# Optimization experiments

Hardware: AMD Instinct MI355X
Metric: run time of the kernel (lower is better)

The kernel has to match this reference:

```python
import math
import jax, jax.numpy as jnp
import numpy as np

B, P, DC, NB, H = 32768, 16, 128, 32, 256
BOUND = 10.0
MIN_W = 1e-5
MIN_H = 1e-5
MIN_D = 1e-5
L2PI = 0.5 * math.log(2.0 * math.pi)


def setup_inputs() -> dict:
    key = jax.random.key(0)
    k0, k1, k2, k3 = jax.random.split(key, 4)
    x = jax.random.normal(k0, (B, P, 4), jnp.float32)
    c = jax.random.normal(k1, (B, P, DC), jnp.float32)
    W1 = jax.random.normal(k2, (DC, H), jnp.float32) / np.float32(np.sqrt(DC))
    b1 = jnp.zeros((H,), jnp.float32)
    # small init so spline params start near-identity-ish (typical subnet init)
    W2 = jax.random.normal(k3, (H, 3 * NB + 1), jnp.float32) * np.float32(0.1 / np.sqrt(H))
    b2 = jnp.zeros((3 * NB + 1,), jnp.float32)
    return {"x": x, "c": c, "W1": W1, "b1": b1, "W2": W2, "b2": b2}


def _pad_left_zero(a):
    # pad a zero at the start of the last axis
    pads = [(0, 0)] * (a.ndim - 1) + [(1, 0)]
    return jnp.pad(a, pads)


def _rqs_forward(x, theta):
    """Unconstrained rational-quadratic spline, forward direction.
    x: (B, P); theta: (B, P, 3*NB+1). Returns (z, log|det|), each (B, P)."""
    left, right, bottom, top = -BOUND, BOUND, -BOUND, BOUND
    inside = (x >= left) & (x <= right)

    uw = theta[..., :NB]
    uh = theta[..., NB:2 * NB]
    ud = theta[..., 2 * NB:]  # (B, P, NB+1)

    widths = MIN_W + (1.0 - MIN_W * NB) * jax.nn.softmax(uw, axis=-1)
    cumw = (right - left) * _pad_left_zero(jnp.cumsum(widths, axis=-1)) + left
    cumw = cumw.at[..., 0].set(left).at[..., -1].set(right)
    widths = cumw[..., 1:] - cumw[..., :-1]

    heights = MIN_H + (1.0 - MIN_H * NB) * jax.nn.softmax(uh, axis=-1)
    cumh = (top - bottom) * _pad_left_zero(jnp.cumsum(heights, axis=-1)) + bottom
    cumh = cumh.at[..., 0].set(bottom).at[..., -1].set(top)
    heights = cumh[..., 1:] - cumh[..., :-1]

    derivs = MIN_D + jax.nn.softplus(ud)  # (B, P, NB+1)

    xs = jnp.clip(x, left, right)
    # bin search: index of the bin containing xs
    bin_idx = jnp.clip(jnp.sum(xs[..., None] >= cumw, axis=-1) - 1, 0, NB - 1)
    idx = bin_idx[..., None]

    def g(a):
        return jnp.take_along_axis(a, idx, axis=-1)[..., 0]

    in_cw = g(cumw[..., :-1])
    in_w = g(widths)
    in_ch = g(cumh[..., :-1])
    in_h = g(heights)
    d0 = g(derivs[..., :-1])
    d1 = g(derivs[..., 1:])
    delta = in_h / in_w

    th = (xs - in_cw) / in_w
    th_om = th * (1.0 - th)
    numerator = in_h * (delta * th * th + d0 * th_om)
    denominator = delta + (d0 + d1 - 2.0 * delta) * th_om
    out = in_ch + numerator / denominator

    deriv_num = delta * delta * (d1 * th * th + 2.0 * delta * th_om + d0 * (1.0 - th) ** 2)
    logabsdet = jnp.log(deriv_num) - 2.0 * jnp.log(denominator)

    z = jnp.where(inside, out, x)
    jac = jnp.where(inside, logabsdet, jnp.zeros_like(x))
    return z, jac


def reference(x, c, W1, b1, W2, b2):
    # subnet MLP: c (B, P, DC) -> theta (B, P, 3*NB+1)
    h = jax.nn.relu(jnp.einsum("bpd,dh->bph", c, W1) + b1)
    theta = jnp.einsum("bph,hk->bpk", h, W2) + b2
    z, jac = _rqs_forward(x[..., -1], theta)
    prob = -L2PI - 0.5 * z * z + jac  # (B, P)
    return prob.sum(axis=1)  # (B,)
```

## Files before the change

### kernel.cpp

```cpp
#include <hip/hip_runtime.h>
#include <math.h>

#define NBLK 256
#define NTHR 512
#define PAIRS 8

typedef float  f32x4  __attribute__((ext_vector_type(4)));
typedef float  f32x16 __attribute__((ext_vector_type(16)));
typedef __bf16 bf16x8 __attribute__((ext_vector_type(8)));
typedef unsigned int u32x4 __attribute__((ext_vector_type(4)));

#define W1S 272
#define W2S 528
#define LDS_W1T 0
#define LDS_W2T 69632
#define LDS_B1  137216
#define LDS_B2  138240
#define LDS_TOTAL 138752

#define L2PIF 0.9189385332046727f
#define AW (1.0f - 32.0f*1e-5f)
#define LOG2E 1.4426950408889634f
#define LN2F  0.6931471805599453f

__device__ __forceinline__ void mfma_v(f32x16& acc, bf16x8 a, bf16x8 b) {
    asm("s_nop 1\n\tv_mfma_f32_32x32x16_bf16 %0, %1, %2, %0"
        : "+v"(acc) : "v"(a), "v"(b));
}
__device__ __forceinline__ void mfma_v_f(f32x16& acc, bf16x8 a, bf16x8 b) {
    asm("v_mfma_f32_32x32x16_bf16 %0, %1, %2, %0"
        : "+v"(acc) : "v"(a), "v"(b));
}
__device__ __forceinline__ void mfma_a_f(f32x16& acc, bf16x8 a, bf16x8 b) {
    asm("v_mfma_f32_32x32x16_bf16 %0, %1, %2, %0"
        : "+a"(acc) : "v"(a), "v"(b));
}
__device__ __forceinline__ void mfma_a_n(f32x16& acc, bf16x8 a, bf16x8 b) {
    asm("s_nop 1\n\tv_mfma_f32_32x32x16_bf16 %0, %1, %2, %0"
        : "+a"(acc) : "v"(a), "v"(b));
}
__device__ __forceinline__ void mfma_a_init(f32x16& acc, bf16x8 a, bf16x8 b) {
    asm("v_mfma_f32_32x32x16_bf16 %0, %1, %2, 0"
        : "=a"(acc) : "v"(a), "v"(b));
}
__device__ __forceinline__ void mfma_a_init_n(f32x16& acc, bf16x8 a, bf16x8 b) {
    asm("s_nop 1\n\tv_mfma_f32_32x32x16_bf16 %0, %1, %2, 0"
        : "=a"(acc) : "v"(a), "v"(b));
}
__device__ __forceinline__ void mfma_fence_va(f32x16& v0, f32x16& a1) {
    asm("s_nop 7\n\ts_nop 7\n\ts_nop 7" : "+v"(v0), "+a"(a1));
}
__device__ __forceinline__ void mfma_fence1(f32x16& a0) {
    asm("s_nop 7\n\ts_nop 7\n\ts_nop 7" : "+a"(a0));
}
__device__ __forceinline__ void mfma_fence2aa(f32x16& a0, f32x16& a1) {
    asm("s_nop 7\n\ts_nop 7\n\ts_nop 7" : "+a"(a0), "+a"(a1));
}

__device__ __forceinline__ void pl32swap(unsigned &a, unsigned &b) {
#if __has_builtin(__builtin_amdgcn_permlane32_swap)
    auto r = __builtin_amdgcn_permlane32_swap(a, b, false, false);
    a = (unsigned)r[0]; b = (unsigned)r[1];
#else
    asm("v_permlane32_swap_b32 %0, %1" : "+v"(a), "+v"(b));
#endif
}
__device__ __forceinline__ float sum32(float x) {
    unsigned a = __float_as_uint(x), b = a;
    pl32swap(a, b);
    return __uint_as_float(a) + __uint_as_float(b);
}
__device__ __forceinline__ float part32(float x) {
    unsigned u = __float_as_uint(x), a = u, b = u;
    pl32swap(a, b);
    return __uint_as_float(a ^ b ^ u);
}

__device__ __forceinline__ float rcpf(float x) {
#if __has_builtin(__builtin_amdgcn_rcpf)
    return __builtin_amdgcn_rcpf(x);
#else
    return 1.f / x;
#endif
}
__device__ __forceinline__ float exp2f_i(float x) {
#if __has_builtin(__builtin_amdgcn_exp2f)
    return __builtin_amdgcn_exp2f(x);
#else
    return __expf(x * LN2F);
#endif
}
__device__ __forceinline__ float log2f_i(float x) {
#if __has_builtin(__builtin_amdgcn_logf)
    return __builtin_amdgcn_logf(x);
#else
    return __logf(x) * LOG2E;
#endif
}
__device__ __forceinline__ float softplus2(float up) {
    return fmaxf(up, 0.f) + log2f_i(1.f + exp2f_i(-fabsf(up)));
}

template<int CTRL>
__device__ __forceinline__ float dppf(float v) {
    return __int_as_float(__builtin_amdgcn_update_dpp(
        0, __float_as_int(v), CTRL, 0xF, 0xF, false));
}
__device__ __forceinline__ float rorsum16(float x) {
    x += dppf<0x121>(x);
    x += dppf<0x122>(x);
    x += dppf<0x124>(x);
    x += dppf<0x128>(x);
    return x;
}
__device__ __forceinline__ unsigned packbf(float a, float b) {
    unsigned short ua = __builtin_bit_cast(unsigned short, (__bf16)a);
    unsigned short ub = __builtin_bit_cast(unsigned short, (__bf16)b);
    return (unsigned)ua | ((unsigned)ub << 16);
}
__device__ __forceinline__ bf16x8 cvt8(f32x4 a, f32x4 b) {
    bf16x8 r;
    r[0]=(__bf16)a[0]; r[1]=(__bf16)a[1]; r[2]=(__bf16)a[2]; r[3]=(__bf16)a[3];
    r[4]=(__bf16)b[0]; r[5]=(__bf16)b[1]; r[6]=(__bf16)b[2]; r[7]=(__bf16)b[3];
    return r;
}

__device__ __forceinline__ void cum_softmax(const f32x16& tv, const char* bias,
                                            int h, float hf, float hoff,
                                            float* a, float* pw0)
{
    float bs0, bs1, bs2, bs3;
    #pragma unroll
    for (int m = 0; m < 4; ++m) {
        f32x4 bv = *(const f32x4*)(bias + m*32);
        float e0 = exp2f_i(tv[4*m+0] + bv[0]);
        float e1 = exp2f_i(tv[4*m+1] + bv[1]);
        float e2 = exp2f_i(tv[4*m+2] + bv[2]);
        float e3 = exp2f_i(tv[4*m+3] + bv[3]);
        a[4*m+0] = e0; a[4*m+1] = e1; a[4*m+2] = e2; a[4*m+3] = e3;
        float s = (e0 + e1) + (e2 + e3);
        if (m == 0) bs0 = s; else if (m == 1) bs1 = s;
        else if (m == 2) bs2 = s; else bs3 = s;
    }
    float t0 = sum32(bs0), t1 = sum32(bs1), t2 = sum32(bs2), t3 = sum32(bs3);
    float T1 = t0, T2 = T1 + t1, T3 = T2 + t2, S = T3 + t3;
    float sc = (20.f * AW) * rcpf(S);
    float st0 = hf * (t0 - bs0);
    float st1 = T1 + hf * (t1 - bs1);
    float st2 = T2 + hf * (t2 - bs2);
    float st3 = T3 + hf * (t3 - bs3);
    pw0[0] = fmaf(sc, st0, hoff);
    pw0[1] = fmaf(sc, st1, hoff + 1.6e-3f);
    pw0[2] = fmaf(sc, st2, hoff + 3.2e-3f);
    pw0[3] = fmaf(sc, st3, hoff + 4.8e-3f);
    #pragma unroll
    for (int m = 0; m < 4; ++m) {
        float run = (m == 0) ? st0 : (m == 1) ? st1 : (m == 2) ? st2 : st3;
        #pragma unroll
        for (int e = 0; e < 4; ++e) {
            run += a[4*m+e];
            a[4*m+e] = hoff + fmaf(sc, run, 2.0e-4f*(float)(8*m + e + 1));
        }
    }
    if (h) a[15] = 10.f;
}

__global__ __launch_bounds__(NTHR)
__attribute__((amdgpu_waves_per_eu(2)))
void flow_kernel(const float* __restrict__ x, const float* __restrict__ c,
                 const float* __restrict__ W1, const float* __restrict__ b1,
                 const float* __restrict__ W2, const float* __restrict__ b2,
                 float* __restrict__ out)
{
    extern __shared__ char smem[];
    const int tid  = threadIdx.x;
    const int wave = tid >> 6;
    const int lane = tid & 63;
    const int p    = lane & 31;
    const int h    = lane >> 5;
    const float hf   = (float)h;
    const float hoff = h ? (8.0e-4f - 10.f) : -10.f;

    {
        const f32x4* W1v = (const f32x4*)W1;
        for (int it = 0; it < 16; ++it) {
            int f4i = tid + it*NTHR;
            int d  = f4i >> 6;
            int j0 = (f4i & 63) << 2;
            f32x4 v = W1v[f4i];
            #pragma unroll
            for (int e = 0; e < 4; ++e) {
                int j = j0 + e;
                *(__bf16*)(smem + LDS_W1T + j*W1S + d*2) = (__bf16)v[e];
            }
        }
        const f32x4* W2v = (const f32x4*)W2;
        for (int f4i = tid; f4i < 6208; f4i += NTHR) {
            f32x4 v = W2v[f4i];
            #pragma unroll
            for (int e = 0; e < 4; ++e) {
                int lin = f4i*4 + e;
                int j = lin / 97;
                int q = lin - j*97;
                *(__bf16*)(smem + LDS_W2T + q*W2S + j*2) = (__bf16)(v[e] * LOG2E);
            }
        }
        for (int i = tid; i < 31*256; i += NTHR) {
            int q = 97 + (i >> 8);
            int j = i & 255;
            *(__bf16*)(smem + LDS_W2T + q*W2S + j*2) = (__bf16)0.f;
        }
        float* b1s = (float*)(smem + LDS_B1);
        float* b2s = (float*)(smem + LDS_B2);
        if (tid < 256) b1s[tid] = b1[tid];
        if (tid < 128) b2s[tid] = (tid < 97) ? b2[tid] * LOG2E : 0.f;
    }
    __syncthreads();

    const char* w1b = smem + LDS_W1T + p*W1S + h*16;
    const char* w2b = smem + LDS_W2T + p*W2S + h*16;
    const char* bb1 = smem + LDS_B1 + h*16;
    const char* bb2 = smem + LDS_B2 + h*16;
    const float b96v = *(const float*)(smem + LDS_B2 + 384);

    const int base = blockIdx.x*128 + wave*16;

    bf16x8 cfrag[8];
    {
        const float* crow = c + (size_t)(base*16 + p)*128 + h*8;
        #pragma unroll
        for (int s = 0; s < 8; ++s)
            cfrag[s] = cvt8(*(const f32x4*)(crow + s*16),
                            *(const f32x4*)(crow + s*16 + 4));
    }
    float xr = x[(size_t)(base*16 + p)*4 + 3];

    for (int itn = 0; itn < PAIRS; ++itn) {
        const int t0 = base + itn*2;
        const int tn = (itn + 1 < PAIRS) ? (t0 + 2) : t0;
        const float* crow_n = c + (size_t)(tn*16 + p)*128 + h*8;

        f32x16 g2[4];
        f32x4  pf[6];
        bf16x8 cfrag_n[8];

        __builtin_amdgcn_s_setprio(1);

        #pragma unroll
        for (int jt = 0; jt < 8; ++jt) {
            pf[(jt % 3)*2]     = *(const f32x4*)(crow_n + jt*16);
            pf[(jt % 3)*2 + 1] = *(const f32x4*)(crow_n + jt*16 + 4);

            f32x16 g1a;
            #pragma unroll
            for (int m = 0; m < 4; ++m) {
                f32x4 bv = *(const f32x4*)(bb1 + jt*128 + m*32);
                g1a[4*m+0] = bv[0]; g1a[4*m+1] = bv[1];
                g1a[4*m+2] = bv[2]; g1a[4*m+3] = bv[3];
            }
            f32x16 g1b;
            #pragma unroll
            for (int s = 0; s < 4; ++s) {
                bf16x8 wa0 = *(const bf16x8*)(w1b + jt*32*W1S + s*32);
                bf16x8 wa1 = *(const bf16x8*)(w1b + jt*32*W1S + (s+4)*32);
                if (s == 0) { mfma_v(g1a, wa0, cfrag[0]);
                              mfma_a_init(g1b, wa1, cfrag[4]); }
                else        { mfma_v_f(g1a, wa0, cfrag[s]);
                              mfma_a_f(g1b, wa1, cfrag[s+4]); }
            }
            mfma_fence_va(g1a, g1b);
            unsigned P[8];
            #pragma unroll
            for (int m = 0; m < 4; ++m) {
                float v0 = fmaxf(g1a[4*m+0] + g1b[4*m+0], 0.f);
                float v1 = fmaxf(g1a[4*m+1] + g1b[4*m+1], 0.f);
                float v2 = fmaxf(g1a[4*m+2] + g1b[4*m+2], 0.f);
                float v3 = fmaxf(g1a[4*m+3] + g1b[4*m+3], 0.f);
                P[2*m]   = packbf(v0, v1);
                P[2*m+1] = packbf(v2, v3);
            }
            #pragma unroll
            for (int cc = 0; cc < 2; ++cc) {
                unsigned fa = P[4*cc+0], fb = P[4*cc+2];
                pl32swap(fa, fb);
                unsigned fc = P[4*cc+1], fd = P[4*cc+3];
                pl32swap(fc, fd);
                u32x4 fr;
                fr[0] = fa; fr[1] = fc; fr[2] = fb; fr[3] = fd;
                bf16x8 hb = __builtin_bit_cast(bf16x8, fr);
                const int kc = 2*jt + cc;
                #pragma unroll
                for (int qt = 0; qt < 4; ++qt) {
                    bf16x8 wb = *(const bf16x8*)(w2b + qt*32*W2S + kc*32);
                    if (jt == 0 && cc == 0) {
                        if (qt == 0) mfma_a_init_n(g2[qt], wb, hb);
                        else         mfma_a_init(g2[qt], wb, hb);
                    } else {
                        if (qt == 0) mfma_a_n(g2[qt], wb, hb);
                        else         mfma_a_f(g2[qt], wb, hb);
                    }
                }
            }
            if (jt >= 2) {
                const int s = jt - 2;
                cfrag_n[s] = cvt8(pf[(s % 3)*2], pf[(s % 3)*2 + 1]);
            }
        }
        __builtin_amdgcn_s_setprio(0);

        if (itn + 1 < PAIRS) {
            cfrag_n[6] = cvt8(pf[(6 % 3)*2], pf[(6 % 3)*2 + 1]);
            cfrag_n[7] = cvt8(pf[(7 % 3)*2], pf[(7 % 3)*2 + 1]);
        }
        const float xr_cur = xr;
        float xn = x[(size_t)(tn*16 + p)*4 + 3];

        mfma_fence1(g2[0]);
        const float xs = fminf(fmaxf(xr_cur, -10.f), 10.f);
        unsigned selm = 0;
        float a_cw, a_cwp;
        {
            float cw[16], pw0[4];
            float acw[4]  = {0.f, 0.f, 0.f, 0.f};
            float acwp[4] = {0.f, 0.f, 0.f, 0.f};
            cum_softmax(g2[0], bb2, h, hf, hoff, cw, pw0);
            #pragma unroll
            for (int r = 0; r < 16; ++r) {
                const int m = r >> 2;
                float pw = (r & 3) ? cw[r-1] : pw0[m];
                bool sel = (xs >= pw) && ((xs < cw[r]) || (h && r == 15));
                float mf = sel ? 1.f : 0.f;
                acw[m]  = fmaf(mf, pw,    acw[m]);
                acwp[m] = fmaf(mf, cw[r], acwp[m]);
                selm |= (sel ? 1u : 0u) << r;
            }
            a_cw  = sum32((acw[0]  + acw[1])  + (acw[2]  + acw[3]));
            a_cwp = sum32((acwp[0] + acwp[1]) + (acwp[2] + acwp[3]));
        }
        mfma_fence1(g2[1]);
        float a_ch, a_chp;
        {
            float ch[16], ph0[4];
            float ach[4]  = {0.f, 0.f, 0.f, 0.f};
            float achp[4] = {0.f, 0.f, 0.f, 0.f};
            cum_softmax(g2[1], bb2 + 128, h, hf, hoff, ch, ph0);
            #pragma unroll
            for (int r = 0; r < 16; ++r) {
                const int m = r >> 2;
                float ph = (r & 3) ? ch[r-1] : ph0[m];
                float mf = (float)((selm >> r) & 1u);
                ach[m]  = fmaf(mf, ph,    ach[m]);
                achp[m] = fmaf(mf, ch[r], achp[m]);
            }
            a_ch  = sum32((ach[0]  + ach[1])  + (ach[2]  + ach[3]));
            a_chp = sum32((achp[0] + achp[1]) + (achp[2] + achp[3]));
        }
        mfma_fence2aa(g2[2], g2[3]);
        float a_d0, a_d1;
        {
            float rv[16];
            float ad0[4] = {0.f, 0.f, 0.f, 0.f};
            float ad1[4] = {0.f, 0.f, 0.f, 0.f};
            #pragma unroll
            for (int m = 0; m < 4; ++m) {
                f32x4 bv = *(const f32x4*)(bb2 + 256 + m*32);
                #pragma unroll
                for (int e = 0; e < 4; ++e)
                    rv[4*m+e] = g2[2][4*m+e] + bv[e];
            }
            float d32r = g2[3][0] + b96v;
            float Z[4];
            #pragma unroll
            for (int m = 0; m < 4; ++m) Z[m] = part32(rv[4*m]);
            float Z4 = part32(d32r);
            #pragma unroll
            for (int r = 0; r < 16; ++r) {
                const int m = r >> 2;
                float nd = ((r & 3) < 3) ? rv[r+1] : (h ? ((m < 3) ? Z[m+1] : Z4) : Z[m]);
                float mf = (float)((selm >> r) & 1u);
                ad0[m] = fmaf(mf, rv[r], ad0[m]);
                ad1[m] = fmaf(mf, nd,    ad1[m]);
            }
            float u0 = sum32((ad0[0] + ad0[1]) + (ad0[2] + ad0[3]));
            float u1 = sum32((ad1[0] + ad1[1]) + (ad1[2] + ad1[3]));
            a_d0 = fmaf(LN2F, softplus2(u0), 1e-5f);
            a_d1 = fmaf(LN2F, softplus2(u1), 1e-5f);
        }

        float val;
        if (xr_cur >= -10.f && xr_cur <= 10.f) {
            float in_w  = a_cwp - a_cw;
            float in_h  = a_chp - a_ch;
            float rw    = rcpf(in_w);
            float delta = in_h * rw;
            float tt    = (xs - a_cw) * rw;
            float thom  = tt * (1.f - tt);
            float den   = delta + (a_d0 + a_d1 - 2.f*delta)*thom;
            float rden  = rcpf(den);
            float z     = fmaf(in_h*(delta*tt*tt + a_d0*thom), rden, a_ch);
            float omt   = 1.f - tt;
            float dnum  = delta*delta*(a_d1*tt*tt + 2.f*delta*thom + a_d0*omt*omt);
            float lv    = log2f_i(dnum) - 2.f*log2f_i(den);
            val = fmaf(LN2F, lv, -L2PIF - 0.5f*z*z);
        } else {
            val = -L2PIF - 0.5f*xr_cur*xr_cur;
        }

        val = rorsum16(val);
        if (lane == 0)  out[t0]     = val;
        if (lane == 16) out[t0 + 1] = val;

        xr = xn;
        if (itn + 1 < PAIRS) {
            #pragma unroll
            for (int s = 0; s < 8; ++s) cfrag[s] = cfrag_n[s];
        }
    }
}

extern "C" void kernel_launch(void* const* d_in, const int* in_sizes, int n_in,
                              void* d_out, int out_size, void* d_ws, size_t ws_size,
                              hipStream_t stream) {
    (void)in_sizes; (void)n_in; (void)out_size; (void)d_ws; (void)ws_size;
    const float* x  = (const float*)d_in[0];
    const float* c  = (const float*)d_in[1];
    const float* W1 = (const float*)d_in[2];
    const float* b1 = (const float*)d_in[3];
    const float* W2 = (const float*)d_in[4];
    const float* b2 = (const float*)d_in[5];
    float* out = (float*)d_out;

    (void)hipFuncSetAttribute((const void*)flow_kernel,
                              hipFuncAttributeMaxDynamicSharedMemorySize, LDS_TOTAL);

    flow_kernel<<<NBLK, NTHR, LDS_TOTAL, stream>>>(x, c, W1, b1, W2, b2, out);
}
```

Baseline: 94.57 us.

## Use 12 waves per block and drop software prefetch of next c tile

Raises the block to 768 threads (12 waves, waves_per_eu 3) and replaces the fixed per-wave pair loop with a strided slot loop over 64 slots. The register-heavy cross-iteration prefetch of the next c fragment is removed, so each iteration loads and converts its c rows at the start instead. The intent is to hide memory latency through more resident waves instead of explicit prefetch. The trade-off is that load latency is now exposed within each wave, and the work split is uneven: 64 slots over 12 waves gives some waves 6 slots and others 5.

```diff
diff --git a/kernel.cpp b/kernel.cpp
--- a/kernel.cpp
+++ b/kernel.cpp
@@ -2,8 +2,9 @@
 #include <math.h>
 
 #define NBLK 256
-#define NTHR 512
-#define PAIRS 8
+#define NTHR 768
+#define NSLOT 64
+#define NWAVE 12
 
 typedef float  f32x4  __attribute__((ext_vector_type(4)));
 typedef float  f32x16 __attribute__((ext_vector_type(16)));
@@ -166,7 +167,7 @@
 }
 
 __global__ __launch_bounds__(NTHR)
-__attribute__((amdgpu_waves_per_eu(2)))
+__attribute__((amdgpu_waves_per_eu(3)))
 void flow_kernel(const float* __restrict__ x, const float* __restrict__ c,
                  const float* __restrict__ W1, const float* __restrict__ b1,
                  const float* __restrict__ W2, const float* __restrict__ b2,
@@ -183,8 +184,7 @@
 
     {
         const f32x4* W1v = (const f32x4*)W1;
-        for (int it = 0; it < 16; ++it) {
-            int f4i = tid + it*NTHR;
+        for (int f4i = tid; f4i < 8192; f4i += NTHR) {
             int d  = f4i >> 6;
             int j0 = (f4i & 63) << 2;
             f32x4 v = W1v[f4i];
@@ -223,34 +223,33 @@
     const char* bb2 = smem + LDS_B2 + h*16;
     const float b96v = *(const float*)(smem + LDS_B2 + 384);
 
-    const int base = blockIdx.x*128 + wave*16;
-
-    bf16x8 cfrag[8];
-    {
-        const float* crow = c + (size_t)(base*16 + p)*128 + h*8;
-        #pragma unroll
-        for (int s = 0; s < 8; ++s)
-            cfrag[s] = cvt8(*(const f32x4*)(crow + s*16),
-                            *(const f32x4*)(crow + s*16 + 4));
-    }
-    float xr = x[(size_t)(base*16 + p)*4 + 3];
-
-    for (int itn = 0; itn < PAIRS; ++itn) {
-        const int t0 = base + itn*2;
-        const int tn = (itn + 1 < PAIRS) ? (t0 + 2) : t0;
-        const float* crow_n = c + (size_t)(tn*16 + p)*128 + h*8;
+    const int blockBase = blockIdx.x * 128;
+
+    for (int slot = wave; slot < NSLOT; slot += NWAVE) {
+        const int t0 = blockBase + slot*2;
+        const float* crow = c + (size_t)(t0*16 + p)*128 + h*8;
+
+        const float xr_cur = x[(size_t)(t0*16 + p)*4 + 3];
+
+        bf16x8 cfrag[8];
+        {
+            f32x4 L[16];
+            #pragma unroll
+            for (int s = 0; s < 8; ++s) {
+                L[2*s]   = *(const f32x4*)(crow + s*16);
+                L[2*s+1] = *(const f32x4*)(crow + s*16 + 4);
+            }
+            #pragma unroll
+            for (int s = 0; s < 8; ++s)
+                cfrag[s] = cvt8(L[2*s], L[2*s+1]);
+        }
 
         f32x16 g2[4];
-        f32x4  pf[6];
-        bf16x8 cfrag_n[8];
 
         __builtin_amdgcn_s_setprio(1);
 
         #pragma unroll
         for (int jt = 0; jt < 8; ++jt) {
-            pf[(jt % 3)*2]     = *(const f32x4*)(crow_n + jt*16);
-            pf[(jt % 3)*2 + 1] = *(const f32x4*)(crow_n + jt*16 + 4);
-
             f32x16 g1a;
             #pragma unroll
             for (int m = 0; m < 4; ++m) {
@@ -301,19 +300,8 @@
                     }
                 }
             }
-            if (jt >= 2) {
-                const int s = jt - 2;
-                cfrag_n[s] = cvt8(pf[(s % 3)*2], pf[(s % 3)*2 + 1]);
-            }
         }
         __builtin_amdgcn_s_setprio(0);
-
-        if (itn + 1 < PAIRS) {
-            cfrag_n[6] = cvt8(pf[(6 % 3)*2], pf[(6 % 3)*2 + 1]);
-            cfrag_n[7] = cvt8(pf[(7 % 3)*2], pf[(7 % 3)*2 + 1]);
-        }
-        const float xr_cur = xr;
-        float xn = x[(size_t)(tn*16 + p)*4 + 3];
 
         mfma_fence1(g2[0]);
         const float xs = fminf(fmaxf(xr_cur, -10.f), 10.f);
@@ -409,12 +397,6 @@
         val = rorsum16(val);
         if (lane == 0)  out[t0]     = val;
         if (lane == 16) out[t0 + 1] = val;
-
-        xr = xn;
-        if (itn + 1 < PAIRS) {
-            #pragma unroll
-            for (int s = 0; s < 8; ++s) cfrag[s] = cfrag_n[s];
-        }
     }
 }
 
```

New measurement: 97.56 us. +3.2%, slower.
